# Kernel tuning notes

Hardware: AMD Instinct MI355X
Metric: run time of the kernel (lower is better)

## Reference

```python
import jax, jax.numpy as jnp
import numpy as np

N_NODES = 50000
N_EDGES = 1000000
D_FEAT = 512
F_ATTN = 64
SLOPE = 0.2


def setup_inputs() -> dict:
    key = jax.random.key(0)
    ks = jax.random.split(key, 8)
    d_sim = jax.random.normal(ks[0], (N_NODES, D_FEAT), dtype=jnp.float32)
    m_sim = jax.random.normal(ks[1], (N_NODES, D_FEAT), dtype=jnp.float32)
    Wd = jax.random.normal(ks[2], (F_ATTN, D_FEAT), dtype=jnp.float32) * (1.0 / np.sqrt(D_FEAT))
    Wm = jax.random.normal(ks[3], (F_ATTN, D_FEAT), dtype=jnp.float32) * (1.0 / np.sqrt(D_FEAT))
    Wa = jax.random.normal(ks[4], (2 * F_ATTN,), dtype=jnp.float32) * (1.0 / np.sqrt(2 * F_ATTN))
    node_type = jax.random.randint(ks[5], (N_NODES,), 0, 2, dtype=jnp.int32)
    edge_src = jax.random.randint(ks[6], (N_EDGES,), 0, N_NODES, dtype=jnp.int32)
    edge_dst = jax.random.randint(ks[7], (N_EDGES,), 0, N_NODES, dtype=jnp.int32)
    return {"d_sim": d_sim, "m_sim": m_sim, "Wd": Wd, "Wm": Wm, "Wa": Wa,
            "node_type": node_type, "edge_src": edge_src, "edge_dst": edge_dst}


def reference(d_sim, m_sim, Wd, Wm, Wa, node_type, edge_src, edge_dst):
    # Per-node projection, type-dependent (type==1 -> disease fc, type==0 -> miRNA fc).
    # Dropout is 0.0 (identity).
    z_d = d_sim @ Wd.T                      # [N, F]
    z_m = m_sim @ Wm.T                      # [N, F]
    z = jnp.where(node_type[:, None] == 1, z_d, z_m)  # [N, F]

    # Edge attention: a = attn_fc(concat(z_src, z_dst)); split Wa to avoid materializing concat.
    zs = z[edge_src]                        # [E, F]
    e = zs @ Wa[:F_ATTN] + z[edge_dst] @ Wa[F_ATTN:]  # [E]
    e = jax.nn.leaky_relu(e, negative_slope=SLOPE)

    # Segment softmax over incoming edges of each dst node (DGL mailbox softmax).
    emax = jax.ops.segment_max(e, edge_dst, num_segments=N_NODES)  # [N]
    ex = jnp.exp(e - emax[edge_dst])                                # [E]
    denom = jax.ops.segment_sum(ex, edge_dst, num_segments=N_NODES)  # [N]
    alpha = ex / denom[edge_dst]                                    # [E]

    # Weighted neighbor aggregation + elu.
    h = jax.ops.segment_sum(alpha[:, None] * zs, edge_dst, num_segments=N_NODES)  # [N, F]
    return jax.nn.elu(h)
```

## Files before the change

kernel.cpp:

```cpp
#include <hip/hip_runtime.h>
#include <hip/hip_bf16.h>

#define N_NODES 50000
#define N_EDGES 1000000
#define D_FEAT 512
#define F_ATTN 64
#define SLOPE 0.2f
#define CAP 64
#define BINS 391
#define BINCAP 4096
#define NPROJ 782
#define NBINBLK 489
#define EPB2 2048
#define NB_TOT (NPROJ + NBINBLK)

typedef __attribute__((ext_vector_type(8))) short short8;
typedef __attribute__((ext_vector_type(4))) float floatx4;

static __device__ __forceinline__ short f2bf(float x) {
    unsigned u = __float_as_uint(x);
    unsigned r = (u + 0x7FFFu + ((u >> 16) & 1u)) >> 16;
    return (short)r;
}

static __device__ __forceinline__ short8 cvt2(float4 x, float4 y) {
    short8 r;
    r[0] = f2bf(x.x); r[1] = f2bf(x.y); r[2] = f2bf(x.z); r[3] = f2bf(x.w);
    r[4] = f2bf(y.x); r[5] = f2bf(y.y); r[6] = f2bf(y.z); r[7] = f2bf(y.w);
    return r;
}

static __device__ __forceinline__ float bfu2f(unsigned short v) {
    return __uint_as_float((unsigned)v << 16);
}

static __device__ __forceinline__ void g2lds16(const void* g, void* l) {
    __builtin_amdgcn_global_load_lds(
        (const __attribute__((address_space(1))) void*)g,
        (__attribute__((address_space(3))) void*)l, 16, 0, 0);
}

__global__ __launch_bounds__(256) void wcvt_kernel(
    const float* __restrict__ Wd, const float* __restrict__ Wm,
    short* __restrict__ Wb, int* __restrict__ gcount)
{
    int i = blockIdx.x * 256 + threadIdx.x;
    int half = F_ATTN * D_FEAT;
    float v = (i < half) ? Wd[i] : Wm[i - half];
    Wb[i] = f2bf(v);
    if (i < BINS) gcount[i] = 0;
}

__global__ __launch_bounds__(256) void fused_kernel(
    const float* __restrict__ d_sim,
    const float* __restrict__ m_sim,
    const short* __restrict__ Wb,
    const float* __restrict__ Wa,
    const int* __restrict__ node_type,
    const int* __restrict__ edge_src,
    const int* __restrict__ edge_dst,
    __hip_bfloat16* __restrict__ z,
    float* __restrict__ s1, float* __restrict__ s2,
    int* __restrict__ gcount, int* __restrict__ bins)
{
    __shared__ char smem[65536];

    const int bid = blockIdx.x;
    const int tid = threadIdx.x;
    const int r13 = bid % 13;
    const int nbBefore = (bid / 13) * 5 + (r13 < 5 ? r13 : 5);
    const bool isBin = (r13 < 5) && (nbBefore < NBINBLK);

    if (isBin) {
        int* hist = (int*)smem;
        int* base = (int*)(smem + 4096);
        const int q = nbBefore;
        for (int i = tid; i < BINS; i += 256) hist[i] = 0;
        __syncthreads();

        int e0 = q * EPB2 + tid * 8;
        int myV[8], myB[8], myR[8];
        if (e0 + 8 <= N_EDGES) {
            int4 d0 = *(const int4*)(edge_dst + e0);
            int4 d1 = *(const int4*)(edge_dst + e0 + 4);
            int4 s0 = *(const int4*)(edge_src + e0);
            int4 s1v = *(const int4*)(edge_src + e0 + 4);
            int dd[8] = {d0.x, d0.y, d0.z, d0.w, d1.x, d1.y, d1.z, d1.w};
            int ss[8] = {s0.x, s0.y, s0.z, s0.w, s1v.x, s1v.y, s1v.z, s1v.w};
            #pragma unroll
            for (int k = 0; k < 8; k++) {
                myV[k] = (ss[k] << 7) | (dd[k] & 127);
                myB[k] = dd[k] >> 7;
                myR[k] = atomicAdd(&hist[myB[k]], 1);
            }
        } else {
            #pragma unroll
            for (int k = 0; k < 8; k++) {
                int e = e0 + k;
                if (e < N_EDGES) {
                    int d = edge_dst[e];
                    int s = edge_src[e];
                    myV[k] = (s << 7) | (d & 127);
                    myB[k] = d >> 7;
                    myR[k] = atomicAdd(&hist[myB[k]], 1);
                } else { myV[k] = -1; myB[k] = 0; myR[k] = 0; }
            }
        }
        __syncthreads();
        for (int i = tid; i < BINS; i += 256) {
            int c = hist[i];
            base[i] = c ? atomicAdd(&gcount[i], c) : 0;
        }
        __syncthreads();
        #pragma unroll
        for (int k = 0; k < 8; k++) {
            if (myV[k] >= 0) {
                int pos = base[myB[k]] + myR[k];
                if (pos < BINCAP) bins[(myB[k] << 12) + pos] = myV[k];
            }
        }
        return;
    }

    const int p      = bid - (nbBefore < NBINBLK ? nbBefore : NBINBLK);
    const int w      = tid >> 6;
    const int lane   = tid & 63;
    const int laneLo = lane & 15;
    const int quad   = lane >> 4;
    const int nodeBase = p * 64;

    const float* aP[4];
    #pragma unroll
    for (int i = 0; i < 4; i++) {
        int r = w * 16 + i * 4 + (lane >> 4);
        int arow = nodeBase + r; if (arow >= N_NODES) arow = N_NODES - 1;
        int lc = (lane & 15) ^ (r & 7);
        const float* src = (node_type[arow] == 1) ? d_sim : m_sim;
        aP[i] = src + (size_t)arow * D_FEAT + (lc << 2);
    }
    const short* bP[4];
    #pragma unroll
    for (int i = 0; i < 4; i++) {
        int r = (w * 4 + i) * 8 + (lane >> 3);
        int lc = (lane & 7) ^ (r & 7);
        bP[i] = Wb + (size_t)r * D_FEAT + (lc << 3);
    }

    floatx4 accD[4], accM[4];
    #pragma unroll
    for (int nt = 0; nt < 4; nt++) {
        accD[nt] = (floatx4){0.f, 0.f, 0.f, 0.f};
        accM[nt] = (floatx4){0.f, 0.f, 0.f, 0.f};
    }

    {
        char* b0 = smem;
        #pragma unroll
        for (int i = 0; i < 4; i++)
            g2lds16(aP[i], b0 + (w * 16 + i * 4) * 256);
        #pragma unroll
        for (int i = 0; i < 4; i++)
            g2lds16(bP[i], b0 + 16384 + (w * 4 + i) * 1024);
    }
    __syncthreads();

    const int rA  = w * 16 + laneLo;
    const int rx  = laneLo & 7;

    for (int t = 0; t < 8; t++) {
        if (t < 7) {
            char* nb = smem + ((t + 1) & 1) * 32768;
            int k0 = (t + 1) * 64;
            #pragma unroll
            for (int i = 0; i < 4; i++)
                g2lds16(aP[i] + k0, nb + (w * 16 + i * 4) * 256);
            #pragma unroll
            for (int i = 0; i < 4; i++)
                g2lds16(bP[i] + k0, nb + 16384 + (w * 4 + i) * 1024);
        }
        const char* cb = smem + (t & 1) * 32768;
        #pragma unroll
        for (int ks = 0; ks < 2; ks++) {
            int c0 = ks * 8 + quad * 2;
            float4 a0 = *(const float4*)(cb + rA * 256 + ((c0 ^ rx) << 4));
            float4 a1 = *(const float4*)(cb + rA * 256 + (((c0 + 1) ^ rx) << 4));
            short8 a = cvt2(a0, a1);
            int ch = ks * 4 + quad;
            int sl = (ch ^ rx) << 4;
            #pragma unroll
            for (int nt = 0; nt < 4; nt++) {
                const char* rowD = cb + 16384 + (nt * 16 + laneLo) * 128;
                short8 bD = *(const short8*)(rowD + sl);
                short8 bM = *(const short8*)(rowD + 64 * 128 + sl);
                accD[nt] = __builtin_amdgcn_mfma_f32_16x16x32_bf16(a, bD, accD[nt], 0, 0, 0);
                accM[nt] = __builtin_amdgcn_mfma_f32_16x16x32_bf16(a, bM, accM[nt], 0, 0, 0);
            }
        }
        __syncthreads();
    }

    float wa1[4], wa2[4];
    #pragma unroll
    for (int nt = 0; nt < 4; nt++) {
        wa1[nt] = Wa[nt * 16 + laneLo];
        wa2[nt] = Wa[F_ATTN + nt * 16 + laneLo];
    }

    #pragma unroll
    for (int reg = 0; reg < 4; reg++) {
        int node = nodeBase + w * 16 + quad * 4 + reg;
        bool ok = node < N_NODES;
        int isD = ok ? (node_type[node] == 1) : 0;
        float p1 = 0.f, p2 = 0.f;
        #pragma unroll
        for (int nt = 0; nt < 4; nt++) {
            float v = isD ? accD[nt][reg] : accM[nt][reg];
            if (ok) z[(size_t)node * F_ATTN + nt * 16 + laneLo] = __float2bfloat16(v);
            p1 += v * wa1[nt];
            p2 += v * wa2[nt];
        }
        #pragma unroll
        for (int off = 8; off; off >>= 1) {
            p1 += __shfl_xor(p1, off);
            p2 += __shfl_xor(p2, off);
        }
        if (ok && laneLo == 0) { s1[node] = p1; s2[node] = p2; }
    }
}

__global__ __launch_bounds__(1024) void agg_kernel(
    const int* __restrict__ gcount, const int* __restrict__ bins,
    const float* __restrict__ s1, const float* __restrict__ s2,
    const __hip_bfloat16* __restrict__ z, float* __restrict__ out)
{
    __shared__ unsigned short list[128 * CAP];
    __shared__ int lcnt[128];
    __shared__ float sW[16 * 64];
    __shared__ int   sS[16 * 64];
    int tid = threadIdx.x;
    int b   = blockIdx.x;
    if (tid < 128) lcnt[tid] = 0;
    __syncthreads();

    int bc = gcount[b]; if (bc > BINCAP) bc = BINCAP;
    for (int i = tid; i < bc; i += 1024) {
        int v = bins[(b << 12) + i];
        int n = v & 127;
        int s = v >> 7;
        int r = atomicAdd(&lcnt[n], 1);
        if (r < CAP) list[(n << 6) + r] = (unsigned short)s;
    }
    __syncthreads();

    int wv    = tid >> 6;
    int lane  = tid & 63;
    int fgrp  = (lane & 15) * 4;
    int ep    = lane >> 4;
    int wbase = wv * 64;

    for (int j8 = 0; j8 < 8; j8++) {
        int ln   = wv * 8 + j8;
        int node = (b << 7) + ln;
        bool nvalid = node < N_NODES;
        int cnt = nvalid ? lcnt[ln] : 0;
        if (cnt > CAP) cnt = CAP;

        int   src = 0;
        float wgt = 0.f;
        if (lane < cnt) {
            src = list[(ln << 6) + lane];
            float t = s1[src] + s2[node];
            float ev = (t > 0.f) ? t : SLOPE * t;
            wgt = __expf(ev);
        }
        float l = wgt;
        sW[wbase + lane] = wgt;
        sS[wbase + lane] = src;

        float4 h = {0.f, 0.f, 0.f, 0.f};
        int usteps = (cnt + 3) >> 2;
        for (int uu = 0; uu < usteps; uu++) {
            int slot = wbase + (uu << 2) + ep;
            float wj = sW[slot];
            int   sj = sS[slot];
            ushort4 zz = *(const ushort4*)((const unsigned short*)z +
                                           (size_t)sj * F_ATTN + fgrp);
            h.x += wj * bfu2f(zz.x);
            h.y += wj * bfu2f(zz.y);
            h.z += wj * bfu2f(zz.z);
            h.w += wj * bfu2f(zz.w);
        }
        #pragma unroll
        for (int off = 16; off <= 32; off <<= 1) {
            h.x += __shfl_xor(h.x, off);
            h.y += __shfl_xor(h.y, off);
            h.z += __shfl_xor(h.z, off);
            h.w += __shfl_xor(h.w, off);
        }
        #pragma unroll
        for (int off = 32; off; off >>= 1) l += __shfl_xor(l, off);

        if (ep == 0 && nvalid) {
            float inv = (cnt > 0) ? 1.f / l : 0.f;
            float4 o;
            float v;
            v = h.x * inv; o.x = (v > 0.f) ? v : (__expf(v) - 1.f);
            v = h.y * inv; o.y = (v > 0.f) ? v : (__expf(v) - 1.f);
            v = h.z * inv; o.z = (v > 0.f) ? v : (__expf(v) - 1.f);
            v = h.w * inv; o.w = (v > 0.f) ? v : (__expf(v) - 1.f);
            *(float4*)(out + (size_t)node * F_ATTN + fgrp) = o;
        }
    }
}

extern "C" void kernel_launch(void* const* d_in, const int* in_sizes, int n_in,
                              void* d_out, int out_size, void* d_ws, size_t ws_size,
                              hipStream_t stream) {
    const float* d_sim = (const float*)d_in[0];
    const float* m_sim = (const float*)d_in[1];
    const float* Wd    = (const float*)d_in[2];
    const float* Wm    = (const float*)d_in[3];
    const float* Wa    = (const float*)d_in[4];
    const int* node_type = (const int*)d_in[5];
    const int* edge_src  = (const int*)d_in[6];
    const int* edge_dst  = (const int*)d_in[7];
    float* out = (float*)d_out;

    char* ws = (char*)d_ws;
    __hip_bfloat16* z  = (__hip_bfloat16*)(ws + 0);
    float* s1          = (float*)(ws + 6400000);
    float* s2          = (float*)(ws + 6600000);
    int*   gcount      = (int*)  (ws + 6800000);
    short* Wb          = (short*)(ws + 7000000);
    int*   bins        = (int*)  (ws + 8388608);

    wcvt_kernel<<<(2 * F_ATTN * D_FEAT) / 256, 256, 0, stream>>>(Wd, Wm, Wb, gcount);
    fused_kernel<<<NB_TOT, 256, 0, stream>>>(
        d_sim, m_sim, Wb, Wa, node_type, edge_src, edge_dst,
        z, s1, s2, gcount, bins);
    agg_kernel<<<BINS, 1024, 0, stream>>>(gcount, bins, s1, s2, z, out);
}
```

Measured before the change: 253.9 us.

## Batch edge-weight computation for all eight nodes per wave and unroll gather loop

```diff
diff --git a/kernel.cpp b/kernel.cpp
--- a/kernel.cpp
+++ b/kernel.cpp
@@ -234,11 +234,14 @@
     const __hip_bfloat16* __restrict__ z, float* __restrict__ out)
 {
     __shared__ unsigned short list[128 * CAP];
+    __shared__ float sW[128 * CAP];
     __shared__ int lcnt[128];
-    __shared__ float sW[16 * 64];
-    __shared__ int   sS[16 * 64];
     int tid = threadIdx.x;
     int b   = blockIdx.x;
+
+    unsigned int* lz = (unsigned int*)list;
+    #pragma unroll
+    for (int i = 0; i < 4; i++) lz[tid + i * 1024] = 0u;
     if (tid < 128) lcnt[tid] = 0;
     __syncthreads();
 
@@ -256,39 +259,56 @@
     int lane  = tid & 63;
     int fgrp  = (lane & 15) * 4;
     int ep    = lane >> 4;
-    int wbase = wv * 64;
-
+
+    int   cnt8[8];
+    float sv8[8];
+    #pragma unroll
+    for (int j8 = 0; j8 < 8; j8++) {
+        int ln = wv * 8 + j8;
+        int c = lcnt[ln]; if (c > CAP) c = CAP;
+        cnt8[j8] = c;
+        int src = list[(ln << 6) + lane];
+        sv8[j8] = s1[src];
+    }
+    float l8[8];
+    #pragma unroll
+    for (int j8 = 0; j8 < 8; j8++) {
+        int ln = wv * 8 + j8;
+        int node = (b << 7) + ln;
+        int nc = (node < N_NODES) ? node : 0;
+        float t = sv8[j8] + s2[nc];
+        float ev = (t > 0.f) ? t : SLOPE * t;
+        float wgt = (lane < cnt8[j8]) ? __expf(ev) : 0.f;
+        sW[(ln << 6) + lane] = wgt;
+        l8[j8] = wgt;
+    }
+    #pragma unroll
+    for (int off = 32; off; off >>= 1) {
+        #pragma unroll
+        for (int j8 = 0; j8 < 8; j8++)
+            l8[j8] += __shfl_xor(l8[j8], off);
+    }
+
+    #pragma unroll
     for (int j8 = 0; j8 < 8; j8++) {
         int ln   = wv * 8 + j8;
         int node = (b << 7) + ln;
-        bool nvalid = node < N_NODES;
-        int cnt = nvalid ? lcnt[ln] : 0;
-        if (cnt > CAP) cnt = CAP;
-
-        int   src = 0;
-        float wgt = 0.f;
-        if (lane < cnt) {
-            src = list[(ln << 6) + lane];
-            float t = s1[src] + s2[node];
-            float ev = (t > 0.f) ? t : SLOPE * t;
-            wgt = __expf(ev);
-        }
-        float l = wgt;
-        sW[wbase + lane] = wgt;
-        sS[wbase + lane] = src;
+        int cnt  = cnt8[j8];
 
         float4 h = {0.f, 0.f, 0.f, 0.f};
-        int usteps = (cnt + 3) >> 2;
-        for (int uu = 0; uu < usteps; uu++) {
-            int slot = wbase + (uu << 2) + ep;
-            float wj = sW[slot];
-            int   sj = sS[slot];
-            ushort4 zz = *(const ushort4*)((const unsigned short*)z +
-                                           (size_t)sj * F_ATTN + fgrp);
-            h.x += wj * bfu2f(zz.x);
-            h.y += wj * bfu2f(zz.y);
-            h.z += wj * bfu2f(zz.z);
-            h.w += wj * bfu2f(zz.w);
+        for (int j = 0; j < cnt; j += 16) {
+            #pragma unroll
+            for (int u = 0; u < 16; u += 4) {
+                int slot = (ln << 6) + j + u + ep;
+                float wj = sW[slot];
+                int   sj = list[slot];
+                ushort4 zz = *(const ushort4*)((const unsigned short*)z +
+                                               (size_t)sj * F_ATTN + fgrp);
+                h.x += wj * bfu2f(zz.x);
+                h.y += wj * bfu2f(zz.y);
+                h.z += wj * bfu2f(zz.z);
+                h.w += wj * bfu2f(zz.w);
+            }
         }
         #pragma unroll
         for (int off = 16; off <= 32; off <<= 1) {
@@ -297,11 +317,9 @@
             h.z += __shfl_xor(h.z, off);
             h.w += __shfl_xor(h.w, off);
         }
-        #pragma unroll
-        for (int off = 32; off; off >>= 1) l += __shfl_xor(l, off);
-
-        if (ep == 0 && nvalid) {
-            float inv = (cnt > 0) ? 1.f / l : 0.f;
+
+        if (ep == 0 && node < N_NODES) {
+            float inv = (cnt > 0) ? 1.f / l8[j8] : 0.f;
             float4 o;
             float v;
             v = h.x * inv; o.x = (v > 0.f) ? v : (__expf(v) - 1.f);
```

Measured after the change: 259.0 us. 2.0% more time.

## Split aggregation across two blocks per bin by feature half

Applied to the files above, without the earlier changes.

```diff
diff --git a/kernel.cpp b/kernel.cpp
--- a/kernel.cpp
+++ b/kernel.cpp
@@ -13,6 +13,7 @@
 #define NBINBLK 489
 #define EPB2 2048
 #define NB_TOT (NPROJ + NBINBLK)
+#define NAGG 784
 
 typedef __attribute__((ext_vector_type(8))) short short8;
 typedef __attribute__((ext_vector_type(4))) float floatx4;
@@ -234,11 +235,15 @@
     const __hip_bfloat16* __restrict__ z, float* __restrict__ out)
 {
     __shared__ unsigned short list[128 * CAP];
+    __shared__ float sW[128 * CAP];
     __shared__ int lcnt[128];
-    __shared__ float sW[16 * 64];
-    __shared__ int   sS[16 * 64];
-    int tid = threadIdx.x;
-    int b   = blockIdx.x;
+    int tid  = threadIdx.x;
+    int grp  = blockIdx.x >> 3;
+    int r8   = blockIdx.x & 7;
+    int half = r8 >> 2;
+    int b    = grp * 4 + (r8 & 3);
+    if (b >= BINS) return;
+
     if (tid < 128) lcnt[tid] = 0;
     __syncthreads();
 
@@ -247,60 +252,56 @@
         int v = bins[(b << 12) + i];
         int n = v & 127;
         int s = v >> 7;
-        int r = atomicAdd(&lcnt[n], 1);
-        if (r < CAP) list[(n << 6) + r] = (unsigned short)s;
+        int rk = atomicAdd(&lcnt[n], 1);
+        if (rk < CAP) list[(n << 6) + rk] = (unsigned short)s;
     }
     __syncthreads();
 
-    int wv    = tid >> 6;
-    int lane  = tid & 63;
-    int fgrp  = (lane & 15) * 4;
-    int ep    = lane >> 4;
-    int wbase = wv * 64;
+    int wv   = tid >> 6;
+    int lane = tid & 63;
+    int fo   = half * 32 + (lane & 7) * 4;
+    int ep   = lane >> 3;
 
     for (int j8 = 0; j8 < 8; j8++) {
         int ln   = wv * 8 + j8;
         int node = (b << 7) + ln;
-        bool nvalid = node < N_NODES;
-        int cnt = nvalid ? lcnt[ln] : 0;
+        bool nv  = node < N_NODES;
+        int cnt  = nv ? lcnt[ln] : 0;
         if (cnt > CAP) cnt = CAP;
 
-        int   src = 0;
         float wgt = 0.f;
         if (lane < cnt) {
-            src = list[(ln << 6) + lane];
+            int src = list[(ln << 6) + lane];
             float t = s1[src] + s2[node];
             float ev = (t > 0.f) ? t : SLOPE * t;
             wgt = __expf(ev);
         }
+        sW[(ln << 6) + lane] = wgt;
         float l = wgt;
-        sW[wbase + lane] = wgt;
-        sS[wbase + lane] = src;
+        #pragma unroll
+        for (int off = 32; off; off >>= 1) l += __shfl_xor(l, off);
 
         float4 h = {0.f, 0.f, 0.f, 0.f};
-        int usteps = (cnt + 3) >> 2;
-        for (int uu = 0; uu < usteps; uu++) {
-            int slot = wbase + (uu << 2) + ep;
-            float wj = sW[slot];
-            int   sj = sS[slot];
+        for (int j = 0; j < cnt; j += 8) {
+            int sl = (ln << 6) + j + ep;
+            float wj = sW[sl];
+            int   sj = (j + ep < cnt) ? (int)list[sl] : 0;
             ushort4 zz = *(const ushort4*)((const unsigned short*)z +
-                                           (size_t)sj * F_ATTN + fgrp);
+                                           (size_t)sj * F_ATTN + fo);
             h.x += wj * bfu2f(zz.x);
             h.y += wj * bfu2f(zz.y);
             h.z += wj * bfu2f(zz.z);
             h.w += wj * bfu2f(zz.w);
         }
         #pragma unroll
-        for (int off = 16; off <= 32; off <<= 1) {
+        for (int off = 8; off <= 32; off <<= 1) {
             h.x += __shfl_xor(h.x, off);
             h.y += __shfl_xor(h.y, off);
             h.z += __shfl_xor(h.z, off);
             h.w += __shfl_xor(h.w, off);
         }
-        #pragma unroll
-        for (int off = 32; off; off >>= 1) l += __shfl_xor(l, off);
-
-        if (ep == 0 && nvalid) {
+
+        if (ep == 0 && nv) {
             float inv = (cnt > 0) ? 1.f / l : 0.f;
             float4 o;
             float v;
@@ -308,7 +309,7 @@
             v = h.y * inv; o.y = (v > 0.f) ? v : (__expf(v) - 1.f);
             v = h.z * inv; o.z = (v > 0.f) ? v : (__expf(v) - 1.f);
             v = h.w * inv; o.w = (v > 0.f) ? v : (__expf(v) - 1.f);
-            *(float4*)(out + (size_t)node * F_ATTN + fgrp) = o;
+            *(float4*)(out + (size_t)node * F_ATTN + fo) = o;
         }
     }
 }
@@ -338,5 +339,5 @@
     fused_kernel<<<NB_TOT, 256, 0, stream>>>(
         d_sim, m_sim, Wb, Wa, node_type, edge_src, edge_dst,
         z, s1, s2, gcount, bins);
-    agg_kernel<<<BINS, 1024, 0, stream>>>(gcount, bins, s1, s2, z, out);
-}
+    agg_kernel<<<NAGG, 1024, 0, stream>>>(gcount, bins, s1, s2, z, out);
+}
```

New measurement: 274.7 us. +8.2%, slower.
